# Optimization experiments

Measured on AMD Instinct MI355X. Metric: run time of the kernel, lower is better.

The kernel has to match this reference:

```python
import jax, jax.numpy as jnp
import numpy as np

DT_RANK = 64
D_STATE = 16


def setup_inputs() -> dict:
    key = jax.random.key(0)
    ks = jax.random.split(key, 6)
    B, L, Di = 2, 2048, 2048
    x = jax.random.normal(ks[0], (B, L, Di), dtype=jnp.float32)
    W_xproj = jax.random.normal(ks[1], (DT_RANK + 2 * D_STATE, Di), dtype=jnp.float32) * (Di ** -0.5)
    W_dt = jax.random.uniform(ks[2], (Di, DT_RANK), dtype=jnp.float32, minval=-(DT_RANK ** -0.5), maxval=DT_RANK ** -0.5)
    dt = jnp.exp(jax.random.uniform(ks[3], (Di,), dtype=jnp.float32) * (np.log(0.1) - np.log(0.001)) + np.log(0.001))
    b_dt = dt + jnp.log(-jnp.expm1(-dt))
    A_log = jnp.log(jnp.broadcast_to(jnp.arange(1, D_STATE + 1, dtype=jnp.float32), (Di, D_STATE)))
    D_param = jnp.ones((Di,), dtype=jnp.float32)
    return {"x": x, "W_xproj": W_xproj, "W_dt": W_dt, "b_dt": b_dt, "A_log": A_log, "D_param": D_param}


def _selective_scan(u, delta, A, Bm, Cm):
    # u, delta: (b, l, d); A: (d, n); Bm, Cm: (b, l, n)
    deltaA = jnp.exp(delta[..., None] * A[None, None])          # (b, l, d, n)
    deltaB_u = delta[..., None] * Bm[:, :, None, :] * u[..., None]  # (b, l, d, n)

    def step(h, inp):
        dA, dBu, c = inp                      # dA,dBu: (b,d,n); c: (b,n)
        h = dA * h + dBu
        y = jnp.einsum('bdn,bn->bd', h, c)
        return h, y

    b, l, d = u.shape
    h0 = jnp.zeros((b, d, A.shape[1]), dtype=u.dtype)
    xs = (jnp.moveaxis(deltaA, 1, 0), jnp.moveaxis(deltaB_u, 1, 0), jnp.moveaxis(Cm, 1, 0))
    _, ys = jax.lax.scan(step, h0, xs)        # ys: (l, b, d)
    return jnp.moveaxis(ys, 0, 1)


def reference(x, W_xproj, W_dt, b_dt, A_log, D_param):
    x_dbl = jnp.einsum('bld,ed->ble', x, W_xproj)  # (b, l, dt_rank + 2*n)
    dlt = x_dbl[..., :DT_RANK]
    Bm = x_dbl[..., DT_RANK:DT_RANK + D_STATE]
    Cm = x_dbl[..., DT_RANK + D_STATE:]
    delta = jax.nn.softplus(jnp.einsum('blr,dr->bld', dlt, W_dt) + b_dt)
    A = -jnp.exp(A_log.astype(jnp.float32))
    y = _selective_scan(x, delta, A, Bm, Cm)
    return y + x * D_param[None, None, :]
```

## Files before the change

### kernel.cpp

```cpp
#include <hip/hip_runtime.h>

#define BATCH 2
#define L_SEQ 2048
#define DI 2048
#define NROW (BATCH * L_SEQ)
#define E_DIM 96
#define RNK 64
#define NST 16
#define NCH 64
#define CL 32
#define SPLITK 16
#define KSL (DI / SPLITK)

#define WS_XDBL 0
#define WS_PART 393216
#define WS_HLOC 393216
#define WS_DSUM (393216 + 4194304)
#define WS_HENT (393216 + 6291456)

__device__ __forceinline__ float softplusf(float z) {
    return fmaxf(z, 0.f) + __logf(1.f + __expf(-fabsf(z)));
}

__device__ __forceinline__ void barrier_lds() {
    asm volatile("s_waitcnt lgkmcnt(0)" ::: "memory");
    __builtin_amdgcn_s_barrier();
}

__global__ __launch_bounds__(256) void gemm_xproj_part(const float* __restrict__ x,
                                                       const float* __restrict__ Wx,
                                                       float* __restrict__ part) {
    __shared__ float xs[32][68];
    __shared__ float wsh[32][100];
    const int tid = threadIdx.x;
    const int r0 = blockIdx.x * 64;
    const int kbase0 = blockIdx.y * KSL;
    const int rg = tid >> 4;
    const int cg = tid & 15;

    float acc[4][6];
#pragma unroll
    for (int i = 0; i < 4; i++)
#pragma unroll
        for (int j = 0; j < 6; j++) acc[i][j] = 0.f;

    for (int kt = 0; kt < KSL / 32; kt++) {
        const int kb = kbase0 + kt * 32;
#pragma unroll
        for (int rep = 0; rep < 2; rep++) {
            int i = rep * 256 + tid;
            int row = i >> 3;
            int kq = i & 7;
            float4 v = *(const float4*)&x[(long)(r0 + row) * DI + kb + kq * 4];
            xs[kq * 4 + 0][row] = v.x;
            xs[kq * 4 + 1][row] = v.y;
            xs[kq * 4 + 2][row] = v.z;
            xs[kq * 4 + 3][row] = v.w;
        }
#pragma unroll
        for (int rep = 0; rep < 3; rep++) {
            int i = rep * 256 + tid;
            int e = i >> 3;
            int kq = i & 7;
            float4 v = *(const float4*)&Wx[(long)e * DI + kb + kq * 4];
            wsh[kq * 4 + 0][e] = v.x;
            wsh[kq * 4 + 1][e] = v.y;
            wsh[kq * 4 + 2][e] = v.z;
            wsh[kq * 4 + 3][e] = v.w;
        }
        __syncthreads();
#pragma unroll 8
        for (int k = 0; k < 32; k++) {
            float xr[4], wr[6];
#pragma unroll
            for (int i = 0; i < 4; i++) xr[i] = xs[k][rg * 4 + i];
#pragma unroll
            for (int j = 0; j < 6; j++) wr[j] = wsh[k][cg * 6 + j];
#pragma unroll
            for (int i = 0; i < 4; i++)
#pragma unroll
                for (int j = 0; j < 6; j++) acc[i][j] = fmaf(xr[i], wr[j], acc[i][j]);
        }
        __syncthreads();
    }
    const long sbase = (long)blockIdx.y * NROW * E_DIM;
#pragma unroll
    for (int i = 0; i < 4; i++) {
        long rowb = sbase + (long)(r0 + rg * 4 + i) * E_DIM + cg * 6;
#pragma unroll
        for (int j = 0; j < 6; j++) part[rowb + j] = acc[i][j];
    }
}

__global__ __launch_bounds__(256) void xproj_reduce(const float* __restrict__ part,
                                                    float* __restrict__ xdbl) {
    const int i4 = blockIdx.x * 256 + threadIdx.x;
    const float4* p4 = (const float4*)part;
    float4 s = p4[i4];
#pragma unroll
    for (int sp = 1; sp < SPLITK; sp++) {
        float4 v = p4[(long)sp * (NROW * E_DIM / 4) + i4];
        s.x += v.x; s.y += v.y; s.z += v.z; s.w += v.w;
    }
    ((float4*)xdbl)[i4] = s;
}

#define PW 260
#define PD 36
__global__ __launch_bounds__(256) void gemm_dt_scan(const float* __restrict__ x,
                                                    const float* __restrict__ xdbl,
                                                    const float* __restrict__ Wdt,
                                                    const float* __restrict__ b_dt,
                                                    const float* __restrict__ A_log,
                                                    float* __restrict__ delta,
                                                    float* __restrict__ hloc,
                                                    float* __restrict__ dsumb) {
    __shared__ float region[32 * PW + 32 * PD];
    __shared__ float bsm[CL * NST];
    float* wt  = region;
    float* dlb = region + 32 * PW;
    float* dtt = region;

    const int tid = threadIdx.x;
    const int d0 = blockIdx.x * 256;
    const int c = blockIdx.y;
    const int b = blockIdx.z;
    const int row0 = b * L_SEQ + c * CL;
    const int d = d0 + tid;
    const int rg = tid >> 6;
    const int cg = tid & 63;

    if (tid < 128) {
        int r = tid >> 2, q = tid & 3;
        ((float4*)bsm)[tid] = *(const float4*)&xdbl[(long)(row0 + r) * E_DIM + 64 + q * 4];
    }

    float acc[8][4];
#pragma unroll
    for (int i = 0; i < 8; i++)
#pragma unroll
        for (int j = 0; j < 4; j++) acc[i][j] = 0.f;

    float xv[CL];
    float4 av[4];

#pragma unroll
    for (int kt = 0; kt < 2; kt++) {
        const int kb = kt * 32;
#pragma unroll
        for (int rep = 0; rep < 8; rep++) {
            int i = rep * 256 + tid;
            int col = i >> 3, kq = i & 7;
            float4 v = *(const float4*)&Wdt[(long)(d0 + col) * RNK + kb + kq * 4];
            wt[(kq * 4 + 0) * PW + col] = v.x;
            wt[(kq * 4 + 1) * PW + col] = v.y;
            wt[(kq * 4 + 2) * PW + col] = v.z;
            wt[(kq * 4 + 3) * PW + col] = v.w;
        }
        {
            int r = tid >> 3, kq = tid & 7;
            float4 v = *(const float4*)&xdbl[(long)(row0 + r) * E_DIM + kb + kq * 4];
            dlb[(kq * 4 + 0) * PD + r] = v.x;
            dlb[(kq * 4 + 1) * PD + r] = v.y;
            dlb[(kq * 4 + 2) * PD + r] = v.z;
            dlb[(kq * 4 + 3) * PD + r] = v.w;
        }
        if (kt == 0) {
#pragma unroll
            for (int ll = 0; ll < CL; ll++)
                xv[ll] = x[(long)(row0 + ll) * DI + d];
#pragma unroll
            for (int q = 0; q < 4; q++)
                av[q] = *(const float4*)&A_log[(long)d * NST + q * 4];
        }
        barrier_lds();
#pragma unroll 8
        for (int k = 0; k < 32; k++) {
            float4 xa = *(const float4*)&dlb[k * PD + rg * 8];
            float4 xb = *(const float4*)&dlb[k * PD + rg * 8 + 4];
            float4 wv4 = *(const float4*)&wt[k * PW + cg * 4];
            float xr[8] = {xa.x, xa.y, xa.z, xa.w, xb.x, xb.y, xb.z, xb.w};
            float wr[4] = {wv4.x, wv4.y, wv4.z, wv4.w};
#pragma unroll
            for (int i = 0; i < 8; i++)
#pragma unroll
                for (int j = 0; j < 4; j++) acc[i][j] = fmaf(xr[i], wr[j], acc[i][j]);
        }
        barrier_lds();
    }

    float4 bb = *(const float4*)&b_dt[d0 + cg * 4];
#pragma unroll
    for (int i = 0; i < 8; i++) {
        int r = rg * 8 + i;
        float4 o;
        o.x = softplusf(acc[i][0] + bb.x);
        o.y = softplusf(acc[i][1] + bb.y);
        o.z = softplusf(acc[i][2] + bb.z);
        o.w = softplusf(acc[i][3] + bb.w);
        *(float4*)&delta[(long)(row0 + r) * DI + d0 + cg * 4] = o;
        *(float4*)&dtt[r * 256 + cg * 4] = o;
    }

    float A[16];
#pragma unroll
    for (int q = 0; q < 4; q++) {
        A[q * 4 + 0] = -__expf(av[q].x);
        A[q * 4 + 1] = -__expf(av[q].y);
        A[q * 4 + 2] = -__expf(av[q].z);
        A[q * 4 + 3] = -__expf(av[q].w);
    }
    barrier_lds();

    float h[16];
#pragma unroll
    for (int n = 0; n < 16; n++) h[n] = 0.f;
    float dsum = 0.f;
    for (int ll = 0; ll < CL; ll++) {
        float dc = dtt[ll * 256 + tid];
        float du = dc * xv[ll];
#pragma unroll
        for (int q = 0; q < 4; q++) {
            float4 v = *(const float4*)&bsm[ll * NST + q * 4];
            h[q * 4 + 0] = fmaf(__expf(dc * A[q * 4 + 0]), h[q * 4 + 0], du * v.x);
            h[q * 4 + 1] = fmaf(__expf(dc * A[q * 4 + 1]), h[q * 4 + 1], du * v.y);
            h[q * 4 + 2] = fmaf(__expf(dc * A[q * 4 + 2]), h[q * 4 + 2], du * v.z);
            h[q * 4 + 3] = fmaf(__expf(dc * A[q * 4 + 3]), h[q * 4 + 3], du * v.w);
        }
        dsum += dc;
    }
    const long cb = ((long)(b * NCH + c) * DI + d);
#pragma unroll
    for (int q = 0; q < 4; q++)
        *(float4*)&hloc[cb * 16 + q * 4] =
            make_float4(h[q * 4], h[q * 4 + 1], h[q * 4 + 2], h[q * 4 + 3]);
    dsumb[cb] = dsum;
}

__global__ __launch_bounds__(256, 1) void scan_prefix(const float* __restrict__ A_log,
                                                      const float* __restrict__ hloc,
                                                      const float* __restrict__ dsumb,
                                                      float* __restrict__ hent) {
    const int g = blockIdx.x * 256 + threadIdx.x;
    const int n = g & 15;
    const int d = (g >> 4) & (DI - 1);
    const int b = g >> 15;
    const float An = -__expf(A_log[(long)d * NST + n]);
    const long hstr = (long)DI * NST;
    const long hbase = (long)b * NCH * hstr + (long)d * NST + n;
    const long dbase = (long)b * NCH * DI + d;
    float hl[NCH], dsv[NCH];
#pragma unroll
    for (int cc = 0; cc < NCH; cc++) {
        hl[cc] = hloc[hbase + cc * hstr];
        dsv[cc] = dsumb[dbase + cc * DI];
    }
    float e[NCH];
#pragma unroll
    for (int cc = 0; cc < NCH; cc++) e[cc] = __expf(An * dsv[cc]);
    float hc = 0.f;
#pragma unroll
    for (int cc = 0; cc < NCH; cc++) {
        hent[hbase + cc * hstr] = hc;
        hc = fmaf(e[cc], hc, hl[cc]);
    }
}

__global__ __launch_bounds__(256) void scan_out(const float* __restrict__ x,
                                                const float* __restrict__ xdbl,
                                                const float* __restrict__ A_log,
                                                const float* __restrict__ Dp,
                                                const float* __restrict__ hent,
                                                float* __restrict__ out) {
    __shared__ float bsm[CL * NST];
    __shared__ float csm[CL * NST];
    const int tid = threadIdx.x;
    const int d0 = blockIdx.x * 256;
    const int c = blockIdx.y;
    const int b = blockIdx.z;
    const int row0 = b * L_SEQ + c * CL;
    const int d = d0 + tid;

    {
        int i = tid & 127, r = i >> 2, q = i & 3;
        float4 v = *(const float4*)&xdbl[(long)(row0 + r) * E_DIM + 64 + ((tid >> 7) << 4) + q * 4];
        if (tid < 128) ((float4*)bsm)[i] = v;
        else           ((float4*)csm)[i] = v;
    }
    __syncthreads();

    float4 av[4];
#pragma unroll
    for (int q = 0; q < 4; q++)
        av[q] = *(const float4*)&A_log[(long)d * NST + q * 4];
    const long cb = ((long)(b * NCH + c) * DI + d);
    float4 hv[4];
#pragma unroll
    for (int q = 0; q < 4; q++)
        hv[q] = *(const float4*)&hent[cb * 16 + q * 4];
    const float Dd = Dp[d];

    float dv[CL], xv[CL];
#pragma unroll
    for (int ll = 0; ll < CL; ll++) {
        dv[ll] = out[(long)(row0 + ll) * DI + d];
        xv[ll] = x[(long)(row0 + ll) * DI + d];
    }

    float A[16];
#pragma unroll
    for (int q = 0; q < 4; q++) {
        A[q * 4 + 0] = -__expf(av[q].x);
        A[q * 4 + 1] = -__expf(av[q].y);
        A[q * 4 + 2] = -__expf(av[q].z);
        A[q * 4 + 3] = -__expf(av[q].w);
    }
    float h[16];
#pragma unroll
    for (int q = 0; q < 4; q++) {
        h[q * 4 + 0] = hv[q].x; h[q * 4 + 1] = hv[q].y;
        h[q * 4 + 2] = hv[q].z; h[q * 4 + 3] = hv[q].w;
    }

    long idx = (long)row0 * DI + d;
    for (int ll = 0; ll < CL; ll++) {
        float dc = dv[ll];
        float xc = xv[ll];
        float du = dc * xc;
        float y = 0.f;
#pragma unroll
        for (int q = 0; q < 4; q++) {
            float4 v = *(const float4*)&bsm[ll * NST + q * 4];
            float4 w = *(const float4*)&csm[ll * NST + q * 4];
            float e0 = __expf(dc * A[q * 4 + 0]);
            float e1 = __expf(dc * A[q * 4 + 1]);
            float e2 = __expf(dc * A[q * 4 + 2]);
            float e3 = __expf(dc * A[q * 4 + 3]);
            h[q * 4 + 0] = fmaf(e0, h[q * 4 + 0], du * v.x);
            h[q * 4 + 1] = fmaf(e1, h[q * 4 + 1], du * v.y);
            h[q * 4 + 2] = fmaf(e2, h[q * 4 + 2], du * v.z);
            h[q * 4 + 3] = fmaf(e3, h[q * 4 + 3], du * v.w);
            y = fmaf(h[q * 4 + 0], w.x, y);
            y = fmaf(h[q * 4 + 1], w.y, y);
            y = fmaf(h[q * 4 + 2], w.z, y);
            y = fmaf(h[q * 4 + 3], w.w, y);
        }
        out[idx] = fmaf(xc, Dd, y);
        idx += DI;
    }
}

extern "C" void kernel_launch(void* const* d_in, const int* in_sizes, int n_in,
                              void* d_out, int out_size, void* d_ws, size_t ws_size,
                              hipStream_t stream) {
    const float* x    = (const float*)d_in[0];
    const float* Wx   = (const float*)d_in[1];
    const float* Wdt  = (const float*)d_in[2];
    const float* bdt  = (const float*)d_in[3];
    const float* Alog = (const float*)d_in[4];
    const float* Dp   = (const float*)d_in[5];
    float* out = (float*)d_out;
    float* ws = (float*)d_ws;
    float* xdbl  = ws + WS_XDBL;
    float* partb = ws + WS_PART;
    float* hloc  = ws + WS_HLOC;
    float* dsumb = ws + WS_DSUM;
    float* hent  = ws + WS_HENT;

    gemm_xproj_part<<<dim3(NROW / 64, SPLITK), 256, 0, stream>>>(x, Wx, partb);
    xproj_reduce<<<dim3(NROW * E_DIM / 4 / 256), 256, 0, stream>>>(partb, xdbl);
    gemm_dt_scan<<<dim3(DI / 256, NCH, BATCH), 256, 0, stream>>>(x, xdbl, Wdt, bdt, Alog,
                                                                 out, hloc, dsumb);
    scan_prefix<<<dim3(BATCH * DI * NST / 256), 256, 0, stream>>>(Alog, hloc, dsumb, hent);
    scan_out<<<dim3(DI / 256, NCH, BATCH), 256, 0, stream>>>(x, xdbl, Alog, Dp, hent, out);
}
```

Measured before the change: 202.0 us.

## Group chunks per block and split scan states across half-blocks

Each block in the delta-GEMM/local-scan and output-scan kernels now handles four consecutive chunks, so the chunk-level prefix shrinks from 64 to 16 entries. The first kernel uses 512 threads, with each half scanning 8 of the 16 states. It loads the full 64-rank W_dt tile once and double-buffers the dt-rank inputs. The output scan prefetches the next chunk's x and delta into LDS registers. The hloc/hent layout becomes d-contiguous for coalesced prefix access, and split-K drops from 16 to 8. The cost is far fewer blocks (256 per scan kernel), which may leave the GPU underfilled, plus higher register and LDS pressure.

```diff
diff --git a/kernel.cpp b/kernel.cpp
--- a/kernel.cpp
+++ b/kernel.cpp
@@ -7,16 +7,18 @@
 #define E_DIM 96
 #define RNK 64
 #define NST 16
+#define CL 32
 #define NCH 64
-#define CL 32
-#define SPLITK 16
+#define G 4
+#define NG (NCH / G)
+#define SPLITK 8
 #define KSL (DI / SPLITK)
 
 #define WS_XDBL 0
 #define WS_PART 393216
 #define WS_HLOC 393216
-#define WS_DSUM (393216 + 4194304)
-#define WS_HENT (393216 + 6291456)
+#define WS_DSUM (393216 + 1048576)
+#define WS_HENT (393216 + 3145728)
 
 __device__ __forceinline__ float softplusf(float z) {
     return fmaxf(z, 0.f) + __logf(1.f + __expf(-fabsf(z)));
@@ -105,9 +107,9 @@
     ((float4*)xdbl)[i4] = s;
 }
 
-#define PW 260
-#define PD 36
-__global__ __launch_bounds__(256) void gemm_dt_scan(const float* __restrict__ x,
+#define PWC 260
+#define PDC 36
+__global__ __launch_bounds__(512) void gemm_dt_scan(const float* __restrict__ x,
                                                     const float* __restrict__ xdbl,
                                                     const float* __restrict__ Wdt,
                                                     const float* __restrict__ b_dt,
@@ -115,154 +117,171 @@
                                                     float* __restrict__ delta,
                                                     float* __restrict__ hloc,
                                                     float* __restrict__ dsumb) {
-    __shared__ float region[32 * PW + 32 * PD];
-    __shared__ float bsm[CL * NST];
-    float* wt  = region;
-    float* dlb = region + 32 * PW;
-    float* dtt = region;
-
+    __shared__ float wt[RNK * PWC];
+    __shared__ float dlb[2][RNK * PDC];
+    __shared__ float dtt[CL * 256];
+    __shared__ float xsh[CL * 256];
+    __shared__ float bsm[G * CL * NST];
     const int tid = threadIdx.x;
     const int d0 = blockIdx.x * 256;
-    const int c = blockIdx.y;
+    const int g = blockIdx.y;
     const int b = blockIdx.z;
-    const int row0 = b * L_SEQ + c * CL;
-    const int d = d0 + tid;
+    const int row0 = b * L_SEQ + g * (G * CL);
+    const int dcol = tid & 255;
+    const int d = d0 + dcol;
+    const int half = tid >> 8;
     const int rg = tid >> 6;
     const int cg = tid & 63;
 
-    if (tid < 128) {
-        int r = tid >> 2, q = tid & 3;
-        ((float4*)bsm)[tid] = *(const float4*)&xdbl[(long)(row0 + r) * E_DIM + 64 + q * 4];
-    }
-
-    float acc[8][4];
-#pragma unroll
-    for (int i = 0; i < 8; i++)
-#pragma unroll
-        for (int j = 0; j < 4; j++) acc[i][j] = 0.f;
-
-    float xv[CL];
-    float4 av[4];
-
-#pragma unroll
-    for (int kt = 0; kt < 2; kt++) {
-        const int kb = kt * 32;
-#pragma unroll
-        for (int rep = 0; rep < 8; rep++) {
-            int i = rep * 256 + tid;
-            int col = i >> 3, kq = i & 7;
-            float4 v = *(const float4*)&Wdt[(long)(d0 + col) * RNK + kb + kq * 4];
-            wt[(kq * 4 + 0) * PW + col] = v.x;
-            wt[(kq * 4 + 1) * PW + col] = v.y;
-            wt[(kq * 4 + 2) * PW + col] = v.z;
-            wt[(kq * 4 + 3) * PW + col] = v.w;
-        }
-        {
-            int r = tid >> 3, kq = tid & 7;
-            float4 v = *(const float4*)&xdbl[(long)(row0 + r) * E_DIM + kb + kq * 4];
-            dlb[(kq * 4 + 0) * PD + r] = v.x;
-            dlb[(kq * 4 + 1) * PD + r] = v.y;
-            dlb[(kq * 4 + 2) * PD + r] = v.z;
-            dlb[(kq * 4 + 3) * PD + r] = v.w;
-        }
-        if (kt == 0) {
-#pragma unroll
-            for (int ll = 0; ll < CL; ll++)
-                xv[ll] = x[(long)(row0 + ll) * DI + d];
-#pragma unroll
-            for (int q = 0; q < 4; q++)
-                av[q] = *(const float4*)&A_log[(long)d * NST + q * 4];
+    float4 wv[8];
+#pragma unroll
+    for (int rep = 0; rep < 8; rep++) {
+        int i = rep * 512 + tid;
+        int col = i >> 4, kq = i & 15;
+        wv[rep] = *(const float4*)&Wdt[(long)(d0 + col) * RNK + kq * 4];
+    }
+    float4 bv;
+    { int r = tid >> 2, q = tid & 3;
+      bv = *(const float4*)&xdbl[(long)(row0 + r) * E_DIM + 64 + q * 4]; }
+    float4 dv0;
+    { int r = tid >> 4, kq = tid & 15;
+      dv0 = *(const float4*)&xdbl[(long)(row0 + r) * E_DIM + kq * 4]; }
+    float4 av0 = *(const float4*)&A_log[(long)d * NST + half * 8];
+    float4 av1 = *(const float4*)&A_log[(long)d * NST + half * 8 + 4];
+    float4 bb  = *(const float4*)&b_dt[d0 + cg * 4];
+
+#pragma unroll
+    for (int rep = 0; rep < 8; rep++) {
+        int i = rep * 512 + tid;
+        int col = i >> 4, kq = i & 15;
+        wt[(kq * 4 + 0) * PWC + col] = wv[rep].x;
+        wt[(kq * 4 + 1) * PWC + col] = wv[rep].y;
+        wt[(kq * 4 + 2) * PWC + col] = wv[rep].z;
+        wt[(kq * 4 + 3) * PWC + col] = wv[rep].w;
+    }
+    { int r = tid >> 2, q = tid & 3;
+      *(float4*)&bsm[r * NST + q * 4] = bv; }
+    { int r = tid >> 4, kq = tid & 15;
+      dlb[0][(kq * 4 + 0) * PDC + r] = dv0.x;
+      dlb[0][(kq * 4 + 1) * PDC + r] = dv0.y;
+      dlb[0][(kq * 4 + 2) * PDC + r] = dv0.z;
+      dlb[0][(kq * 4 + 3) * PDC + r] = dv0.w; }
+
+    float A[8];
+    A[0] = -__expf(av0.x); A[1] = -__expf(av0.y);
+    A[2] = -__expf(av0.z); A[3] = -__expf(av0.w);
+    A[4] = -__expf(av1.x); A[5] = -__expf(av1.y);
+    A[6] = -__expf(av1.z); A[7] = -__expf(av1.w);
+    float h[8];
+#pragma unroll
+    for (int n = 0; n < 8; n++) h[n] = 0.f;
+    float dsum = 0.f;
+
+    barrier_lds();
+
+    for (int cc = 0; cc < G; cc++) {
+        const int cur = cc & 1;
+        const int rowc = row0 + cc * CL;
+        float4 xq[4];
+#pragma unroll
+        for (int rep = 0; rep < 4; rep++) {
+            int i = rep * 512 + tid;
+            int r = i >> 6, dq = i & 63;
+            xq[rep] = *(const float4*)&x[(long)(rowc + r) * DI + d0 + dq * 4];
+        }
+        float4 dvn;
+        if (cc < G - 1) {
+            int r = tid >> 4, kq = tid & 15;
+            dvn = *(const float4*)&xdbl[(long)(rowc + CL + r) * E_DIM + kq * 4];
+        }
+        float acc[4][4];
+#pragma unroll
+        for (int i = 0; i < 4; i++)
+#pragma unroll
+            for (int j = 0; j < 4; j++) acc[i][j] = 0.f;
+#pragma unroll 8
+        for (int k = 0; k < RNK; k++) {
+            float4 xa = *(const float4*)&dlb[cur][k * PDC + rg * 4];
+            float4 wr4 = *(const float4*)&wt[k * PWC + cg * 4];
+            float xr[4] = {xa.x, xa.y, xa.z, xa.w};
+            float wr[4] = {wr4.x, wr4.y, wr4.z, wr4.w};
+#pragma unroll
+            for (int i = 0; i < 4; i++)
+#pragma unroll
+                for (int j = 0; j < 4; j++) acc[i][j] = fmaf(xr[i], wr[j], acc[i][j]);
+        }
+        if (cc < G - 1) {
+            int r = tid >> 4, kq = tid & 15;
+            dlb[cur ^ 1][(kq * 4 + 0) * PDC + r] = dvn.x;
+            dlb[cur ^ 1][(kq * 4 + 1) * PDC + r] = dvn.y;
+            dlb[cur ^ 1][(kq * 4 + 2) * PDC + r] = dvn.z;
+            dlb[cur ^ 1][(kq * 4 + 3) * PDC + r] = dvn.w;
         }
         barrier_lds();
-#pragma unroll 8
-        for (int k = 0; k < 32; k++) {
-            float4 xa = *(const float4*)&dlb[k * PD + rg * 8];
-            float4 xb = *(const float4*)&dlb[k * PD + rg * 8 + 4];
-            float4 wv4 = *(const float4*)&wt[k * PW + cg * 4];
-            float xr[8] = {xa.x, xa.y, xa.z, xa.w, xb.x, xb.y, xb.z, xb.w};
-            float wr[4] = {wv4.x, wv4.y, wv4.z, wv4.w};
-#pragma unroll
-            for (int i = 0; i < 8; i++)
-#pragma unroll
-                for (int j = 0; j < 4; j++) acc[i][j] = fmaf(xr[i], wr[j], acc[i][j]);
+#pragma unroll
+        for (int rep = 0; rep < 4; rep++) {
+            int i = rep * 512 + tid;
+            int r = i >> 6, dq = i & 63;
+            *(float4*)&xsh[r * 256 + dq * 4] = xq[rep];
+        }
+#pragma unroll
+        for (int i = 0; i < 4; i++) {
+            float4 o;
+            o.x = softplusf(acc[i][0] + bb.x);
+            o.y = softplusf(acc[i][1] + bb.y);
+            o.z = softplusf(acc[i][2] + bb.z);
+            o.w = softplusf(acc[i][3] + bb.w);
+            *(float4*)&delta[(long)(rowc + rg * 4 + i) * DI + d0 + cg * 4] = o;
+            *(float4*)&dtt[(rg * 4 + i) * 256 + cg * 4] = o;
         }
         barrier_lds();
-    }
-
-    float4 bb = *(const float4*)&b_dt[d0 + cg * 4];
-#pragma unroll
-    for (int i = 0; i < 8; i++) {
-        int r = rg * 8 + i;
-        float4 o;
-        o.x = softplusf(acc[i][0] + bb.x);
-        o.y = softplusf(acc[i][1] + bb.y);
-        o.z = softplusf(acc[i][2] + bb.z);
-        o.w = softplusf(acc[i][3] + bb.w);
-        *(float4*)&delta[(long)(row0 + r) * DI + d0 + cg * 4] = o;
-        *(float4*)&dtt[r * 256 + cg * 4] = o;
-    }
-
-    float A[16];
-#pragma unroll
-    for (int q = 0; q < 4; q++) {
-        A[q * 4 + 0] = -__expf(av[q].x);
-        A[q * 4 + 1] = -__expf(av[q].y);
-        A[q * 4 + 2] = -__expf(av[q].z);
-        A[q * 4 + 3] = -__expf(av[q].w);
-    }
-    barrier_lds();
-
-    float h[16];
-#pragma unroll
-    for (int n = 0; n < 16; n++) h[n] = 0.f;
-    float dsum = 0.f;
-    for (int ll = 0; ll < CL; ll++) {
-        float dc = dtt[ll * 256 + tid];
-        float du = dc * xv[ll];
-#pragma unroll
-        for (int q = 0; q < 4; q++) {
-            float4 v = *(const float4*)&bsm[ll * NST + q * 4];
-            h[q * 4 + 0] = fmaf(__expf(dc * A[q * 4 + 0]), h[q * 4 + 0], du * v.x);
-            h[q * 4 + 1] = fmaf(__expf(dc * A[q * 4 + 1]), h[q * 4 + 1], du * v.y);
-            h[q * 4 + 2] = fmaf(__expf(dc * A[q * 4 + 2]), h[q * 4 + 2], du * v.z);
-            h[q * 4 + 3] = fmaf(__expf(dc * A[q * 4 + 3]), h[q * 4 + 3], du * v.w);
-        }
-        dsum += dc;
-    }
-    const long cb = ((long)(b * NCH + c) * DI + d);
-#pragma unroll
-    for (int q = 0; q < 4; q++)
-        *(float4*)&hloc[cb * 16 + q * 4] =
-            make_float4(h[q * 4], h[q * 4 + 1], h[q * 4 + 2], h[q * 4 + 3]);
-    dsumb[cb] = dsum;
-}
-
-__global__ __launch_bounds__(256, 1) void scan_prefix(const float* __restrict__ A_log,
-                                                      const float* __restrict__ hloc,
-                                                      const float* __restrict__ dsumb,
-                                                      float* __restrict__ hent) {
-    const int g = blockIdx.x * 256 + threadIdx.x;
-    const int n = g & 15;
-    const int d = (g >> 4) & (DI - 1);
-    const int b = g >> 15;
+        for (int ll = 0; ll < CL; ll++) {
+            float dc = dtt[ll * 256 + dcol];
+            float xc = xsh[ll * 256 + dcol];
+            float du = dc * xc;
+            float4 v0 = *(const float4*)&bsm[(cc * CL + ll) * NST + half * 8];
+            float4 v1 = *(const float4*)&bsm[(cc * CL + ll) * NST + half * 8 + 4];
+            h[0] = fmaf(__expf(dc * A[0]), h[0], du * v0.x);
+            h[1] = fmaf(__expf(dc * A[1]), h[1], du * v0.y);
+            h[2] = fmaf(__expf(dc * A[2]), h[2], du * v0.z);
+            h[3] = fmaf(__expf(dc * A[3]), h[3], du * v0.w);
+            h[4] = fmaf(__expf(dc * A[4]), h[4], du * v1.x);
+            h[5] = fmaf(__expf(dc * A[5]), h[5], du * v1.y);
+            h[6] = fmaf(__expf(dc * A[6]), h[6], du * v1.z);
+            h[7] = fmaf(__expf(dc * A[7]), h[7], du * v1.w);
+            dsum += dc;
+        }
+    }
+    const long gb = (long)(b * NG + g);
+#pragma unroll
+    for (int j = 0; j < 8; j++)
+        hloc[(gb * NST + half * 8 + j) * DI + d] = h[j];
+    if (half == 0) dsumb[gb * DI + d] = dsum;
+}
+
+__global__ __launch_bounds__(256) void scan_prefix(const float* __restrict__ A_log,
+                                                   const float* __restrict__ hloc,
+                                                   const float* __restrict__ dsumb,
+                                                   float* __restrict__ hent) {
+    const int gi = blockIdx.x * 256 + threadIdx.x;
+    const int d = gi & (DI - 1);
+    const int n = (gi >> 11) & 15;
+    const int b = gi >> 15;
     const float An = -__expf(A_log[(long)d * NST + n]);
-    const long hstr = (long)DI * NST;
-    const long hbase = (long)b * NCH * hstr + (long)d * NST + n;
-    const long dbase = (long)b * NCH * DI + d;
-    float hl[NCH], dsv[NCH];
-#pragma unroll
-    for (int cc = 0; cc < NCH; cc++) {
-        hl[cc] = hloc[hbase + cc * hstr];
-        dsv[cc] = dsumb[dbase + cc * DI];
-    }
-    float e[NCH];
-#pragma unroll
-    for (int cc = 0; cc < NCH; cc++) e[cc] = __expf(An * dsv[cc]);
+    float hl[NG], dsv[NG];
+#pragma unroll
+    for (int gg = 0; gg < NG; gg++) {
+        hl[gg]  = hloc[((long)(b * NG + gg) * NST + n) * DI + d];
+        dsv[gg] = dsumb[(long)(b * NG + gg) * DI + d];
+    }
+    float e[NG];
+#pragma unroll
+    for (int gg = 0; gg < NG; gg++) e[gg] = __expf(An * dsv[gg]);
     float hc = 0.f;
 #pragma unroll
-    for (int cc = 0; cc < NCH; cc++) {
-        hent[hbase + cc * hstr] = hc;
-        hc = fmaf(e[cc], hc, hl[cc]);
+    for (int gg = 0; gg < NG; gg++) {
+        hent[((long)(b * NG + gg) * NST + n) * DI + d] = hc;
+        hc = fmaf(e[gg], hc, hl[gg]);
     }
 }
 
@@ -272,42 +291,56 @@
                                                 const float* __restrict__ Dp,
                                                 const float* __restrict__ hent,
                                                 float* __restrict__ out) {
-    __shared__ float bsm[CL * NST];
-    __shared__ float csm[CL * NST];
+    __shared__ float xsh[CL * 256];
+    __shared__ float dsh[CL * 256];
+    __shared__ float bsm[G * CL * NST];
+    __shared__ float csm[G * CL * NST];
     const int tid = threadIdx.x;
     const int d0 = blockIdx.x * 256;
-    const int c = blockIdx.y;
+    const int g = blockIdx.y;
     const int b = blockIdx.z;
-    const int row0 = b * L_SEQ + c * CL;
+    const int row0 = b * L_SEQ + g * (G * CL);
     const int d = d0 + tid;
 
-    {
-        int i = tid & 127, r = i >> 2, q = i & 3;
-        float4 v = *(const float4*)&xdbl[(long)(row0 + r) * E_DIM + 64 + ((tid >> 7) << 4) + q * 4];
-        if (tid < 128) ((float4*)bsm)[i] = v;
-        else           ((float4*)csm)[i] = v;
-    }
-    __syncthreads();
-
+    float4 bq[2], cq[2];
+#pragma unroll
+    for (int rep = 0; rep < 2; rep++) {
+        int i = rep * 256 + tid, r = i >> 2, q = i & 3;
+        bq[rep] = *(const float4*)&xdbl[(long)(row0 + r) * E_DIM + 64 + q * 4];
+        cq[rep] = *(const float4*)&xdbl[(long)(row0 + r) * E_DIM + 80 + q * 4];
+    }
     float4 av[4];
 #pragma unroll
     for (int q = 0; q < 4; q++)
         av[q] = *(const float4*)&A_log[(long)d * NST + q * 4];
-    const long cb = ((long)(b * NCH + c) * DI + d);
-    float4 hv[4];
-#pragma unroll
-    for (int q = 0; q < 4; q++)
-        hv[q] = *(const float4*)&hent[cb * 16 + q * 4];
+    const long gb = (long)(b * NG + g);
+    float hv[16];
+#pragma unroll
+    for (int n = 0; n < 16; n++)
+        hv[n] = hent[(gb * NST + n) * DI + d];
     const float Dd = Dp[d];
-
-    float dv[CL], xv[CL];
-#pragma unroll
-    for (int ll = 0; ll < CL; ll++) {
-        dv[ll] = out[(long)(row0 + ll) * DI + d];
-        xv[ll] = x[(long)(row0 + ll) * DI + d];
-    }
-
-    float A[16];
+    float4 xq[8], dq[8];
+#pragma unroll
+    for (int rep = 0; rep < 8; rep++) {
+        int i = rep * 256 + tid, r = i >> 6, dqc = i & 63;
+        xq[rep] = *(const float4*)&x[(long)(row0 + r) * DI + d0 + dqc * 4];
+        dq[rep] = *(const float4*)&out[(long)(row0 + r) * DI + d0 + dqc * 4];
+    }
+
+#pragma unroll
+    for (int rep = 0; rep < 2; rep++) {
+        int i = rep * 256 + tid, r = i >> 2, q = i & 3;
+        *(float4*)&bsm[r * NST + q * 4] = bq[rep];
+        *(float4*)&csm[r * NST + q * 4] = cq[rep];
+    }
+#pragma unroll
+    for (int rep = 0; rep < 8; rep++) {
+        int i = rep * 256 + tid, r = i >> 6, dqc = i & 63;
+        *(float4*)&xsh[r * 256 + dqc * 4] = xq[rep];
+        *(float4*)&dsh[r * 256 + dqc * 4] = dq[rep];
+    }
+
+    float A[16], h[16];
 #pragma unroll
     for (int q = 0; q < 4; q++) {
         A[q * 4 + 0] = -__expf(av[q].x);
@@ -315,38 +348,58 @@
         A[q * 4 + 2] = -__expf(av[q].z);
         A[q * 4 + 3] = -__expf(av[q].w);
     }
-    float h[16];
-#pragma unroll
-    for (int q = 0; q < 4; q++) {
-        h[q * 4 + 0] = hv[q].x; h[q * 4 + 1] = hv[q].y;
-        h[q * 4 + 2] = hv[q].z; h[q * 4 + 3] = hv[q].w;
-    }
-
-    long idx = (long)row0 * DI + d;
-    for (int ll = 0; ll < CL; ll++) {
-        float dc = dv[ll];
-        float xc = xv[ll];
-        float du = dc * xc;
-        float y = 0.f;
-#pragma unroll
-        for (int q = 0; q < 4; q++) {
-            float4 v = *(const float4*)&bsm[ll * NST + q * 4];
-            float4 w = *(const float4*)&csm[ll * NST + q * 4];
-            float e0 = __expf(dc * A[q * 4 + 0]);
-            float e1 = __expf(dc * A[q * 4 + 1]);
-            float e2 = __expf(dc * A[q * 4 + 2]);
-            float e3 = __expf(dc * A[q * 4 + 3]);
-            h[q * 4 + 0] = fmaf(e0, h[q * 4 + 0], du * v.x);
-            h[q * 4 + 1] = fmaf(e1, h[q * 4 + 1], du * v.y);
-            h[q * 4 + 2] = fmaf(e2, h[q * 4 + 2], du * v.z);
-            h[q * 4 + 3] = fmaf(e3, h[q * 4 + 3], du * v.w);
-            y = fmaf(h[q * 4 + 0], w.x, y);
-            y = fmaf(h[q * 4 + 1], w.y, y);
-            y = fmaf(h[q * 4 + 2], w.z, y);
-            y = fmaf(h[q * 4 + 3], w.w, y);
-        }
-        out[idx] = fmaf(xc, Dd, y);
-        idx += DI;
+#pragma unroll
+    for (int n = 0; n < 16; n++) h[n] = hv[n];
+
+    barrier_lds();
+
+    for (int cc = 0; cc < G; cc++) {
+        const int rowc = row0 + cc * CL;
+        float4 xn[8], dn[8];
+        if (cc < G - 1) {
+#pragma unroll
+            for (int rep = 0; rep < 8; rep++) {
+                int i = rep * 256 + tid, r = i >> 6, dqc = i & 63;
+                xn[rep] = *(const float4*)&x[(long)(rowc + CL + r) * DI + d0 + dqc * 4];
+                dn[rep] = *(const float4*)&out[(long)(rowc + CL + r) * DI + d0 + dqc * 4];
+            }
+        }
+        long idx = (long)rowc * DI + d;
+        for (int ll = 0; ll < CL; ll++) {
+            float dc = dsh[ll * 256 + tid];
+            float xc = xsh[ll * 256 + tid];
+            float du = dc * xc;
+            float y = 0.f;
+#pragma unroll
+            for (int q = 0; q < 4; q++) {
+                float4 v = *(const float4*)&bsm[(cc * CL + ll) * NST + q * 4];
+                float4 w = *(const float4*)&csm[(cc * CL + ll) * NST + q * 4];
+                float e0 = __expf(dc * A[q * 4 + 0]);
+                float e1 = __expf(dc * A[q * 4 + 1]);
+                float e2 = __expf(dc * A[q * 4 + 2]);
+                float e3 = __expf(dc * A[q * 4 + 3]);
+                h[q * 4 + 0] = fmaf(e0, h[q * 4 + 0], du * v.x);
+                h[q * 4 + 1] = fmaf(e1, h[q * 4 + 1], du * v.y);
+                h[q * 4 + 2] = fmaf(e2, h[q * 4 + 2], du * v.z);
+                h[q * 4 + 3] = fmaf(e3, h[q * 4 + 3], du * v.w);
+                y = fmaf(h[q * 4 + 0], w.x, y);
+                y = fmaf(h[q * 4 + 1], w.y, y);
+                y = fmaf(h[q * 4 + 2], w.z, y);
+                y = fmaf(h[q * 4 + 3], w.w, y);
+            }
+            out[idx] = fmaf(xc, Dd, y);
+            idx += DI;
+        }
+        barrier_lds();
+        if (cc < G - 1) {
+#pragma unroll
+            for (int rep = 0; rep < 8; rep++) {
+                int i = rep * 256 + tid, r = i >> 6, dqc = i & 63;
+                *(float4*)&xsh[r * 256 + dqc * 4] = xn[rep];
+                *(float4*)&dsh[r * 256 + dqc * 4] = dn[rep];
+            }
+            barrier_lds();
+        }
     }
 }
 
@@ -369,8 +422,8 @@
 
     gemm_xproj_part<<<dim3(NROW / 64, SPLITK), 256, 0, stream>>>(x, Wx, partb);
     xproj_reduce<<<dim3(NROW * E_DIM / 4 / 256), 256, 0, stream>>>(partb, xdbl);
-    gemm_dt_scan<<<dim3(DI / 256, NCH, BATCH), 256, 0, stream>>>(x, xdbl, Wdt, bdt, Alog,
-                                                                 out, hloc, dsumb);
+    gemm_dt_scan<<<dim3(DI / 256, NG, BATCH), 512, 0, stream>>>(x, xdbl, Wdt, bdt, Alog,
+                                                                out, hloc, dsumb);
     scan_prefix<<<dim3(BATCH * DI * NST / 256), 256, 0, stream>>>(Alog, hloc, dsumb, hent);
-    scan_out<<<dim3(DI / 256, NCH, BATCH), 256, 0, stream>>>(x, xdbl, Alog, Dp, hent, out);
-}
+    scan_out<<<dim3(DI / 256, NG, BATCH), 256, 0, stream>>>(x, xdbl, Alog, Dp, hent, out);
+}
```

After: 234.0 us. +15.9%, slower.

## Replace per-state exps with powers of one exp and use d-contiguous state layout

Applied to the files above, without the earlier changes.

At runtime the scan kernels check whether A_n is (n+1)*A_0, which matches the standard Mamba init. If it is, they compute one exp per step and build the 16 decay factors by repeated multiplication instead of calling 16 exps; otherwise they fall back to the original loop. The hloc, hent and dsum buffers are re-laid out so that d is contiguous, giving coalesced accesses in scan_prefix and scan_out. W_dt is pre-transposed inside the reduce kernel so gemm_dt_scan can load it with float4 into LDS without scattered stores. Building high powers by repeated products adds a small amount of rounding error.

```diff
diff --git a/kernel.cpp b/kernel.cpp
--- a/kernel.cpp
+++ b/kernel.cpp
@@ -17,6 +17,7 @@
 #define WS_HLOC 393216
 #define WS_DSUM (393216 + 4194304)
 #define WS_HENT (393216 + 6291456)
+#define WS_WDTT (393216 + 6291456)
 
 __device__ __forceinline__ float softplusf(float z) {
     return fmaxf(z, 0.f) + __logf(1.f + __expf(-fabsf(z)));
@@ -92,24 +93,39 @@
     }
 }
 
-__global__ __launch_bounds__(256) void xproj_reduce(const float* __restrict__ part,
-                                                    float* __restrict__ xdbl) {
-    const int i4 = blockIdx.x * 256 + threadIdx.x;
-    const float4* p4 = (const float4*)part;
-    float4 s = p4[i4];
-#pragma unroll
-    for (int sp = 1; sp < SPLITK; sp++) {
-        float4 v = p4[(long)sp * (NROW * E_DIM / 4) + i4];
-        s.x += v.x; s.y += v.y; s.z += v.z; s.w += v.w;
-    }
-    ((float4*)xdbl)[i4] = s;
+__global__ __launch_bounds__(256) void xproj_reduce_wt(const float* __restrict__ part,
+                                                       float* __restrict__ xdbl,
+                                                       const float* __restrict__ Wdt,
+                                                       float* __restrict__ wdtT) {
+    if (blockIdx.x < 384) {
+        const int i4 = blockIdx.x * 256 + threadIdx.x;
+        const float4* p4 = (const float4*)part;
+        float4 s = p4[i4];
+#pragma unroll
+        for (int sp = 1; sp < SPLITK; sp++) {
+            float4 v = p4[(long)sp * (NROW * E_DIM / 4) + i4];
+            s.x += v.x; s.y += v.y; s.z += v.z; s.w += v.w;
+        }
+        ((float4*)xdbl)[i4] = s;
+    } else {
+        const int t = (blockIdx.x - 384) * 256 + threadIdx.x;
+        const int base = t * 4;
+        const int r = base >> 11;
+        const int d4 = base & (DI - 1);
+        float4 o;
+        o.x = Wdt[(long)(d4 + 0) * RNK + r];
+        o.y = Wdt[(long)(d4 + 1) * RNK + r];
+        o.z = Wdt[(long)(d4 + 2) * RNK + r];
+        o.w = Wdt[(long)(d4 + 3) * RNK + r];
+        *(float4*)&wdtT[base] = o;
+    }
 }
 
 #define PW 260
 #define PD 36
 __global__ __launch_bounds__(256) void gemm_dt_scan(const float* __restrict__ x,
                                                     const float* __restrict__ xdbl,
-                                                    const float* __restrict__ Wdt,
+                                                    const float* __restrict__ wdtT,
                                                     const float* __restrict__ b_dt,
                                                     const float* __restrict__ A_log,
                                                     float* __restrict__ delta,
@@ -150,12 +166,9 @@
 #pragma unroll
         for (int rep = 0; rep < 8; rep++) {
             int i = rep * 256 + tid;
-            int col = i >> 3, kq = i & 7;
-            float4 v = *(const float4*)&Wdt[(long)(d0 + col) * RNK + kb + kq * 4];
-            wt[(kq * 4 + 0) * PW + col] = v.x;
-            wt[(kq * 4 + 1) * PW + col] = v.y;
-            wt[(kq * 4 + 2) * PW + col] = v.z;
-            wt[(kq * 4 + 3) * PW + col] = v.w;
+            int k = i >> 6, c4 = i & 63;
+            float4 v = *(const float4*)&wdtT[(long)(kb + k) * DI + d0 + c4 * 4];
+            *(float4*)&wt[k * PW + c4 * 4] = v;
         }
         {
             int r = tid >> 3, kq = tid & 7;
@@ -210,31 +223,58 @@
         A[q * 4 + 2] = -__expf(av[q].z);
         A[q * 4 + 3] = -__expf(av[q].w);
     }
+    const float A0 = A[0];
+    bool fast = true;
+#pragma unroll
+    for (int n = 1; n < 16; n++)
+        fast = fast && (fabsf(A[n] - (float)(n + 1) * A0) <= 1e-4f * (float)(n + 1));
     barrier_lds();
 
     float h[16];
 #pragma unroll
     for (int n = 0; n < 16; n++) h[n] = 0.f;
     float dsum = 0.f;
-    for (int ll = 0; ll < CL; ll++) {
-        float dc = dtt[ll * 256 + tid];
-        float du = dc * xv[ll];
-#pragma unroll
-        for (int q = 0; q < 4; q++) {
-            float4 v = *(const float4*)&bsm[ll * NST + q * 4];
-            h[q * 4 + 0] = fmaf(__expf(dc * A[q * 4 + 0]), h[q * 4 + 0], du * v.x);
-            h[q * 4 + 1] = fmaf(__expf(dc * A[q * 4 + 1]), h[q * 4 + 1], du * v.y);
-            h[q * 4 + 2] = fmaf(__expf(dc * A[q * 4 + 2]), h[q * 4 + 2], du * v.z);
-            h[q * 4 + 3] = fmaf(__expf(dc * A[q * 4 + 3]), h[q * 4 + 3], du * v.w);
-        }
-        dsum += dc;
-    }
-    const long cb = ((long)(b * NCH + c) * DI + d);
-#pragma unroll
-    for (int q = 0; q < 4; q++)
-        *(float4*)&hloc[cb * 16 + q * 4] =
-            make_float4(h[q * 4], h[q * 4 + 1], h[q * 4 + 2], h[q * 4 + 3]);
-    dsumb[cb] = dsum;
+    if (fast) {
+        for (int ll = 0; ll < CL; ll++) {
+            float dc = dtt[ll * 256 + tid];
+            float du = dc * xv[ll];
+            float p1 = __expf(dc * A0);
+            float p2 = p1 * p1, p3 = p2 * p1, p4 = p2 * p2, p5 = p3 * p2;
+            float p6 = p3 * p3, p7 = p4 * p3, p8 = p4 * p4, p9 = p5 * p4;
+            float p10 = p5 * p5, p11 = p6 * p5, p12 = p6 * p6, p13 = p7 * p6;
+            float p14 = p7 * p7, p15 = p8 * p7, p16 = p8 * p8;
+            float e_[16] = {p1, p2, p3, p4, p5, p6, p7, p8,
+                            p9, p10, p11, p12, p13, p14, p15, p16};
+#pragma unroll
+            for (int q = 0; q < 4; q++) {
+                float4 v = *(const float4*)&bsm[ll * NST + q * 4];
+                h[q * 4 + 0] = fmaf(e_[q * 4 + 0], h[q * 4 + 0], du * v.x);
+                h[q * 4 + 1] = fmaf(e_[q * 4 + 1], h[q * 4 + 1], du * v.y);
+                h[q * 4 + 2] = fmaf(e_[q * 4 + 2], h[q * 4 + 2], du * v.z);
+                h[q * 4 + 3] = fmaf(e_[q * 4 + 3], h[q * 4 + 3], du * v.w);
+            }
+            dsum += dc;
+        }
+    } else {
+        for (int ll = 0; ll < CL; ll++) {
+            float dc = dtt[ll * 256 + tid];
+            float du = dc * xv[ll];
+#pragma unroll
+            for (int q = 0; q < 4; q++) {
+                float4 v = *(const float4*)&bsm[ll * NST + q * 4];
+                h[q * 4 + 0] = fmaf(__expf(dc * A[q * 4 + 0]), h[q * 4 + 0], du * v.x);
+                h[q * 4 + 1] = fmaf(__expf(dc * A[q * 4 + 1]), h[q * 4 + 1], du * v.y);
+                h[q * 4 + 2] = fmaf(__expf(dc * A[q * 4 + 2]), h[q * 4 + 2], du * v.z);
+                h[q * 4 + 3] = fmaf(__expf(dc * A[q * 4 + 3]), h[q * 4 + 3], du * v.w);
+            }
+            dsum += dc;
+        }
+    }
+    const long cb = (long)(b * NCH + c);
+#pragma unroll
+    for (int n = 0; n < 16; n++)
+        hloc[(cb * NST + n) * DI + d] = h[n];
+    dsumb[cb * DI + d] = dsum;
 }
 
 __global__ __launch_bounds__(256, 1) void scan_prefix(const float* __restrict__ A_log,
@@ -242,18 +282,15 @@
                                                       const float* __restrict__ dsumb,
                                                       float* __restrict__ hent) {
     const int g = blockIdx.x * 256 + threadIdx.x;
-    const int n = g & 15;
-    const int d = (g >> 4) & (DI - 1);
+    const int d = g & (DI - 1);
+    const int n = (g >> 11) & 15;
     const int b = g >> 15;
     const float An = -__expf(A_log[(long)d * NST + n]);
-    const long hstr = (long)DI * NST;
-    const long hbase = (long)b * NCH * hstr + (long)d * NST + n;
-    const long dbase = (long)b * NCH * DI + d;
     float hl[NCH], dsv[NCH];
 #pragma unroll
     for (int cc = 0; cc < NCH; cc++) {
-        hl[cc] = hloc[hbase + cc * hstr];
-        dsv[cc] = dsumb[dbase + cc * DI];
+        hl[cc]  = hloc[((long)(b * NCH + cc) * NST + n) * DI + d];
+        dsv[cc] = dsumb[(long)(b * NCH + cc) * DI + d];
     }
     float e[NCH];
 #pragma unroll
@@ -261,7 +298,7 @@
     float hc = 0.f;
 #pragma unroll
     for (int cc = 0; cc < NCH; cc++) {
-        hent[hbase + cc * hstr] = hc;
+        hent[((long)(b * NCH + cc) * NST + n) * DI + d] = hc;
         hc = fmaf(e[cc], hc, hl[cc]);
     }
 }
@@ -293,11 +330,11 @@
 #pragma unroll
     for (int q = 0; q < 4; q++)
         av[q] = *(const float4*)&A_log[(long)d * NST + q * 4];
-    const long cb = ((long)(b * NCH + c) * DI + d);
-    float4 hv[4];
-#pragma unroll
-    for (int q = 0; q < 4; q++)
-        hv[q] = *(const float4*)&hent[cb * 16 + q * 4];
+    const long cb = (long)(b * NCH + c);
+    float hv[16];
+#pragma unroll
+    for (int n = 0; n < 16; n++)
+        hv[n] = hent[(cb * NST + n) * DI + d];
     const float Dd = Dp[d];
 
     float dv[CL], xv[CL];
@@ -315,38 +352,71 @@
         A[q * 4 + 2] = -__expf(av[q].z);
         A[q * 4 + 3] = -__expf(av[q].w);
     }
+    const float A0 = A[0];
+    bool fast = true;
+#pragma unroll
+    for (int n = 1; n < 16; n++)
+        fast = fast && (fabsf(A[n] - (float)(n + 1) * A0) <= 1e-4f * (float)(n + 1));
     float h[16];
 #pragma unroll
-    for (int q = 0; q < 4; q++) {
-        h[q * 4 + 0] = hv[q].x; h[q * 4 + 1] = hv[q].y;
-        h[q * 4 + 2] = hv[q].z; h[q * 4 + 3] = hv[q].w;
-    }
+    for (int n = 0; n < 16; n++) h[n] = hv[n];
 
     long idx = (long)row0 * DI + d;
-    for (int ll = 0; ll < CL; ll++) {
-        float dc = dv[ll];
-        float xc = xv[ll];
-        float du = dc * xc;
-        float y = 0.f;
-#pragma unroll
-        for (int q = 0; q < 4; q++) {
-            float4 v = *(const float4*)&bsm[ll * NST + q * 4];
-            float4 w = *(const float4*)&csm[ll * NST + q * 4];
-            float e0 = __expf(dc * A[q * 4 + 0]);
-            float e1 = __expf(dc * A[q * 4 + 1]);
-            float e2 = __expf(dc * A[q * 4 + 2]);
-            float e3 = __expf(dc * A[q * 4 + 3]);
-            h[q * 4 + 0] = fmaf(e0, h[q * 4 + 0], du * v.x);
-            h[q * 4 + 1] = fmaf(e1, h[q * 4 + 1], du * v.y);
-            h[q * 4 + 2] = fmaf(e2, h[q * 4 + 2], du * v.z);
-            h[q * 4 + 3] = fmaf(e3, h[q * 4 + 3], du * v.w);
-            y = fmaf(h[q * 4 + 0], w.x, y);
-            y = fmaf(h[q * 4 + 1], w.y, y);
-            y = fmaf(h[q * 4 + 2], w.z, y);
-            y = fmaf(h[q * 4 + 3], w.w, y);
-        }
-        out[idx] = fmaf(xc, Dd, y);
-        idx += DI;
+    if (fast) {
+        for (int ll = 0; ll < CL; ll++) {
+            float dc = dv[ll];
+            float xc = xv[ll];
+            float du = dc * xc;
+            float p1 = __expf(dc * A0);
+            float p2 = p1 * p1, p3 = p2 * p1, p4 = p2 * p2, p5 = p3 * p2;
+            float p6 = p3 * p3, p7 = p4 * p3, p8 = p4 * p4, p9 = p5 * p4;
+            float p10 = p5 * p5, p11 = p6 * p5, p12 = p6 * p6, p13 = p7 * p6;
+            float p14 = p7 * p7, p15 = p8 * p7, p16 = p8 * p8;
+            float e_[16] = {p1, p2, p3, p4, p5, p6, p7, p8,
+                            p9, p10, p11, p12, p13, p14, p15, p16};
+            float y = 0.f;
+#pragma unroll
+            for (int q = 0; q < 4; q++) {
+                float4 v = *(const float4*)&bsm[ll * NST + q * 4];
+                float4 w = *(const float4*)&csm[ll * NST + q * 4];
+                h[q * 4 + 0] = fmaf(e_[q * 4 + 0], h[q * 4 + 0], du * v.x);
+                h[q * 4 + 1] = fmaf(e_[q * 4 + 1], h[q * 4 + 1], du * v.y);
+                h[q * 4 + 2] = fmaf(e_[q * 4 + 2], h[q * 4 + 2], du * v.z);
+                h[q * 4 + 3] = fmaf(e_[q * 4 + 3], h[q * 4 + 3], du * v.w);
+                y = fmaf(h[q * 4 + 0], w.x, y);
+                y = fmaf(h[q * 4 + 1], w.y, y);
+                y = fmaf(h[q * 4 + 2], w.z, y);
+                y = fmaf(h[q * 4 + 3], w.w, y);
+            }
+            out[idx] = fmaf(xc, Dd, y);
+            idx += DI;
+        }
+    } else {
+        for (int ll = 0; ll < CL; ll++) {
+            float dc = dv[ll];
+            float xc = xv[ll];
+            float du = dc * xc;
+            float y = 0.f;
+#pragma unroll
+            for (int q = 0; q < 4; q++) {
+                float4 v = *(const float4*)&bsm[ll * NST + q * 4];
+                float4 w = *(const float4*)&csm[ll * NST + q * 4];
+                float e0 = __expf(dc * A[q * 4 + 0]);
+                float e1 = __expf(dc * A[q * 4 + 1]);
+                float e2 = __expf(dc * A[q * 4 + 2]);
+                float e3 = __expf(dc * A[q * 4 + 3]);
+                h[q * 4 + 0] = fmaf(e0, h[q * 4 + 0], du * v.x);
+                h[q * 4 + 1] = fmaf(e1, h[q * 4 + 1], du * v.y);
+                h[q * 4 + 2] = fmaf(e2, h[q * 4 + 2], du * v.z);
+                h[q * 4 + 3] = fmaf(e3, h[q * 4 + 3], du * v.w);
+                y = fmaf(h[q * 4 + 0], w.x, y);
+                y = fmaf(h[q * 4 + 1], w.y, y);
+                y = fmaf(h[q * 4 + 2], w.z, y);
+                y = fmaf(h[q * 4 + 3], w.w, y);
+            }
+            out[idx] = fmaf(xc, Dd, y);
+            idx += DI;
+        }
     }
 }
 
@@ -366,10 +436,11 @@
     float* hloc  = ws + WS_HLOC;
     float* dsumb = ws + WS_DSUM;
     float* hent  = ws + WS_HENT;
+    float* wdtT  = ws + WS_WDTT;
 
     gemm_xproj_part<<<dim3(NROW / 64, SPLITK), 256, 0, stream>>>(x, Wx, partb);
-    xproj_reduce<<<dim3(NROW * E_DIM / 4 / 256), 256, 0, stream>>>(partb, xdbl);
-    gemm_dt_scan<<<dim3(DI / 256, NCH, BATCH), 256, 0, stream>>>(x, xdbl, Wdt, bdt, Alog,
+    xproj_reduce_wt<<<dim3(384 + 128), 256, 0, stream>>>(partb, xdbl, Wdt, wdtT);
+    gemm_dt_scan<<<dim3(DI / 256, NCH, BATCH), 256, 0, stream>>>(x, xdbl, wdtT, bdt, Alog,
                                                                  out, hloc, dsumb);
     scan_prefix<<<dim3(BATCH * DI * NST / 256), 256, 0, stream>>>(Alog, hloc, dsumb, hent);
     scan_out<<<dim3(DI / 256, NCH, BATCH), 256, 0, stream>>>(x, xdbl, Alog, Dp, hent, out);
```

New measurement: 188.5 us. 1.07x faster.
